# Kernel optimization log

Hardware: AMD Instinct MI355X
Metric: run time of the kernel (lower is better)

## Reference

```python
import jax, jax.numpy as jnp
import numpy as np

N, D_MODEL, D_PE, H = 4096, 512, 16, 8


def setup_inputs() -> dict:
    key = jax.random.key(0)
    ks = jax.random.split(key, 6)
    s = 1.0 / np.sqrt(D_MODEL)
    return {
        "x": jax.random.normal(ks[0], (N, D_MODEL), dtype=jnp.float32),
        "pe": jax.random.normal(ks[1], (N, D_PE), dtype=jnp.float32),
        "w_qkv": jax.random.normal(ks[2], (D_MODEL, 3 * D_MODEL), dtype=jnp.float32) * s,
        "b_qkv": jnp.zeros((3 * D_MODEL,), dtype=jnp.float32),
        "w_pe": jax.random.normal(ks[3], (D_PE, H), dtype=jnp.float32) * (1.0 / np.sqrt(D_PE)),
        "b_pe": jnp.zeros((H,), dtype=jnp.float32),
        "w_out": jax.random.normal(ks[4], (D_MODEL, D_MODEL), dtype=jnp.float32) * s,
        "b_out": jnp.zeros((D_MODEL,), dtype=jnp.float32),
    }


def reference(x, pe, w_qkv, b_qkv, w_pe, b_pe, w_out, b_out):
    n, d = x.shape
    h = w_pe.shape[1]
    hd = d // h
    scale = hd ** -0.5

    qkv = (x @ w_qkv + b_qkv).reshape(n, 3, h, hd)  # [N,3,H,hd]
    q = jnp.transpose(qkv[:, 0], (1, 0, 2))  # [H,N,hd]
    k = jnp.transpose(qkv[:, 1], (1, 0, 2))
    v = jnp.transpose(qkv[:, 2], (1, 0, 2))

    pe_proj = pe @ w_pe + b_pe  # [N,H]
    # bias[h,i,j] = pe_proj[j,h] - pe_proj[i,h]  (matches torch unsqueeze/permute)
    pt = pe_proj.T  # [H,N]
    bias = pt[:, None, :] - pt[:, :, None]  # [H,N,N]

    scores = jnp.einsum('hnd,hmd->hnm', q, k) * scale + bias  # [H,N,N]
    attn = jax.nn.softmax(scores, axis=-1)
    out = jnp.einsum('hnm,hmd->hnd', attn, v)  # [H,N,hd]
    out = jnp.transpose(out, (1, 0, 2)).reshape(n, d)
    return out @ w_out + b_out
```

## Files before the change

### kernel.cpp

```cpp
#include <hip/hip_runtime.h>
#include <stdint.h>
#include <stddef.h>


typedef unsigned short u16;
typedef __attribute__((ext_vector_type(8))) short short8;
typedef __attribute__((ext_vector_type(8))) unsigned short us8;
typedef __attribute__((ext_vector_type(4))) unsigned short us4;
typedef __attribute__((ext_vector_type(4))) float floatx4;

__device__ __forceinline__ u16 f2b(float f) {
  union { float f; uint32_t u; } v; v.f = f;
  uint32_t u = v.u;
  return (u16)((u + 0x7fffu + ((u >> 16) & 1u)) >> 16);
}

__device__ __forceinline__ uint32_t pkbf16(float a, float b) {
  union { float f; uint32_t u; } x, y; x.f = a; y.f = b;
  return __builtin_amdgcn_perm(y.u + 0x8000u, x.u + 0x8000u, 0x07060302u);
}

#if __has_builtin(__builtin_amdgcn_exp2f)
__device__ __forceinline__ float fexp2(float x) { return __builtin_amdgcn_exp2f(x); }
#else
__device__ __forceinline__ float fexp2(float x) { return exp2f(x); }
#endif

__device__ __forceinline__ void gld16(const u16* g, u16* l) {
  __builtin_amdgcn_global_load_lds(
      (const __attribute__((address_space(1))) uint32_t*)(const void*)g,
      (__attribute__((address_space(3))) uint32_t*)(void*)l, 16, 0, 0);
}


__device__ __forceinline__ void tr_tile(const float* __restrict__ in,
                                        u16* __restrict__ out, int R, int C,
                                        int bx, int by, u16 (*tile)[33]) {
  int tx = threadIdx.x & 31, ty = threadIdx.x >> 5;
  int c0 = bx * 32, r0 = by * 32;
#pragma unroll
  for (int i = 0; i < 32; i += 8)
    tile[ty + i][tx] = f2b(in[(size_t)(r0 + ty + i) * C + c0 + tx]);
  __syncthreads();
#pragma unroll
  for (int i = 0; i < 32; i += 8)
    out[(size_t)(c0 + ty + i) * R + r0 + tx] = tile[tx][ty + i];
}

__global__ __launch_bounds__(256) void k_prep(
    const float* __restrict__ x, u16* __restrict__ xb,
    const float* __restrict__ w_qkv, u16* __restrict__ wqkvT,
    const float* __restrict__ w_out, u16* __restrict__ woutT,
    const float* __restrict__ pe, const float* __restrict__ w_pe,
    const float* __restrict__ b_pe, float* __restrict__ peT) {
  __shared__ u16 tile[32][33];
  int b = blockIdx.x;
  if (b < 2048) {
    int i = b * 256 + threadIdx.x;
    float4 v = ((const float4*)x)[i];
    uint2 o = make_uint2(pkbf16(v.x, v.y), pkbf16(v.z, v.w));
    ((uint2*)xb)[i] = o;
  } else if (b < 2816) {
    int idx = b - 2048;
    tr_tile(w_qkv, wqkvT, 512, 1536, idx % 48, idx / 48, tile);
  } else if (b < 3072) {
    int idx = b - 2816;
    tr_tile(w_out, woutT, 512, 512, idx % 16, idx / 16, tile);
  } else {
    int idx = (b - 3072) * 256 + threadIdx.x;
    int h = idx >> 12, n = idx & 4095;
    float acc = b_pe[h];
#pragma unroll
    for (int d = 0; d < 16; ++d) acc = fmaf(pe[n * 16 + d], w_pe[d * 8 + h], acc);
    peT[h * 4096 + n] = acc * 1.4426950408889634f - 16.0f;
  }
}


__global__ __launch_bounds__(512, 6) void k_gemm_qkv(const u16* __restrict__ A,
                                                     const u16* __restrict__ Bt,
                                                     const float* __restrict__ bias,
                                                     u16* __restrict__ qk,
                                                     u16* __restrict__ vtp) {
  __shared__ __align__(16) u16 smem[24576];
  const int tid = threadIdx.x;
  const int lane = tid & 63, wave = tid >> 6;
  const int colx = lane & 15, quad = lane >> 4;
  const int m0 = blockIdx.y * 64, n0 = blockIdx.x * 128;
  const int wm = wave >> 2, wn = wave & 3;
  const int sc = (lane & 7) ^ ((lane >> 3) & 7);
  const floatx4 fz = {0.f, 0.f, 0.f, 0.f};
  floatx4 acc[2][2];
#pragma unroll
  for (int i = 0; i < 2; ++i)
#pragma unroll
    for (int j = 0; j < 2; ++j) acc[i][j] = fz;

#define PREF_QKV(k0, b)                                                       \
  {                                                                           \
    int rowa = wave * 8 + (lane >> 3);                                        \
    gld16(&A[(size_t)(m0 + rowa) * 512 + (k0) + sc * 8],                      \
          &smem[(b) * 4096 + wave * 512 + lane * 8]);                         \
    _Pragma("unroll") for (int c = 0; c < 2; ++c) {                           \
      int rowb = wave * 16 + c * 8 + (lane >> 3);                             \
      gld16(&Bt[(size_t)(n0 + rowb) * 512 + (k0) + sc * 8],                   \
            &smem[8192 + (b) * 8192 + wave * 1024 + c * 512 + lane * 8]);     \
    }                                                                         \
  }

  PREF_QKV(0, 0);
  __syncthreads();
  for (int it = 0; it < 8; ++it) {
    int cur = it & 1;
    if (it < 7) PREF_QKV((it + 1) * 64, cur ^ 1);
    const u16* As = &smem[cur * 4096];
    const u16* Bs = &smem[8192 + cur * 8192];
#pragma unroll
    for (int kk = 0; kk < 2; ++kk) {
      short8 af[2], bf[2];
#pragma unroll
      for (int i = 0; i < 2; ++i) {
        int row = wm * 32 + i * 16 + colx;
        af[i] = *(const short8*)&As[row * 64 + (((kk * 4 + quad) ^ (colx & 7))) * 8];
      }
#pragma unroll
      for (int j = 0; j < 2; ++j) {
        int row = wn * 32 + j * 16 + colx;
        bf[j] = *(const short8*)&Bs[row * 64 + (((kk * 4 + quad) ^ (colx & 7))) * 8];
      }
#pragma unroll
      for (int i = 0; i < 2; ++i)
#pragma unroll
        for (int j = 0; j < 2; ++j)
          acc[i][j] = __builtin_amdgcn_mfma_f32_16x16x32_bf16(af[i], bf[j], acc[i][j], 0, 0, 0);
    }
    __syncthreads();
  }

  const bool isV = (blockIdx.x >= 8);
#pragma unroll
  for (int j = 0; j < 2; ++j) {
    int c = n0 + wn * 32 + j * 16 + colx;
    float bq = bias[c];
    if (!isV) {
#pragma unroll
      for (int i = 0; i < 2; ++i)
#pragma unroll
        for (int r = 0; r < 4; ++r) {
          int row = m0 + wm * 32 + i * 16 + quad * 4 + r;
          qk[(size_t)row * 1024 + c] = f2b(acc[i][j][r] + bq);
        }
    } else {
      int d = c - 1024;
#pragma unroll
      for (int i = 0; i < 2; ++i) {
        us4 o;
#pragma unroll
        for (int r = 0; r < 4; ++r) o[r] = f2b(acc[i][j][r] + bq);
        *(us4*)&vtp[(size_t)d * 4096 + m0 + wm * 32 + quad * 8 + i * 4] = o;
      }
    }
  }
#undef PREF_QKV
}


__global__ __launch_bounds__(512, 4) void k_gemm_out(const u16* __restrict__ A,
                                                     const u16* __restrict__ Bt,
                                                     const float* __restrict__ bias,
                                                     float* __restrict__ Cout) {
  __shared__ __align__(16) u16 smem[16384];
  const int tid = threadIdx.x;
  const int lane = tid & 63, wave = tid >> 6;
  const int colx = lane & 15, quad = lane >> 4;
  const int m0 = blockIdx.y * 64, n0 = blockIdx.x * 64;
  const int wm = wave >> 2, wn = wave & 3;
  const int sc = (lane & 7) ^ ((lane >> 3) & 7);
  const floatx4 fz = {0.f, 0.f, 0.f, 0.f};
  floatx4 acc[2];
  acc[0] = fz; acc[1] = fz;

#define PREF_OUT(k0, b)                                                       \
  {                                                                           \
    int rowa = wave * 8 + (lane >> 3);                                        \
    gld16(&A[(size_t)(m0 + rowa) * 512 + (k0) + sc * 8],                      \
          &smem[(b) * 4096 + wave * 512 + lane * 8]);                         \
    gld16(&Bt[(size_t)(n0 + rowa) * 512 + (k0) + sc * 8],                     \
          &smem[8192 + (b) * 4096 + wave * 512 + lane * 8]);                  \
  }

  PREF_OUT(0, 0);
  __syncthreads();
  for (int it = 0; it < 8; ++it) {
    int cur = it & 1;
    if (it < 7) PREF_OUT((it + 1) * 64, cur ^ 1);
    const u16* As = &smem[cur * 4096];
    const u16* Bs = &smem[8192 + cur * 4096];
#pragma unroll
    for (int kk = 0; kk < 2; ++kk) {
      short8 af[2], bf;
#pragma unroll
      for (int i = 0; i < 2; ++i) {
        int row = wm * 32 + i * 16 + colx;
        af[i] = *(const short8*)&As[row * 64 + (((kk * 4 + quad) ^ (colx & 7))) * 8];
      }
      {
        int row = wn * 16 + colx;
        bf = *(const short8*)&Bs[row * 64 + (((kk * 4 + quad) ^ (colx & 7))) * 8];
      }
#pragma unroll
      for (int i = 0; i < 2; ++i)
        acc[i] = __builtin_amdgcn_mfma_f32_16x16x32_bf16(af[i], bf, acc[i], 0, 0, 0);
    }
    __syncthreads();
  }
  int c = n0 + wn * 16 + colx;
  float bq = bias[c];
#pragma unroll
  for (int i = 0; i < 2; ++i)
#pragma unroll
    for (int r = 0; r < 4; ++r) {
      int row = m0 + wm * 32 + i * 16 + quad * 4 + r;
      Cout[(size_t)row * 512 + c] = acc[i][r] + bq;
    }
#undef PREF_OUT
}


__global__ __launch_bounds__(512, 8) void k_flash(const u16* __restrict__ qk,
                                                  const u16* __restrict__ vt,
                                                  const float* __restrict__ peT,
                                                  float* __restrict__ opart,
                                                  float* __restrict__ lpart) {
  __shared__ __align__(16) u16 smem[20480];
  float* bufs = (float*)smem;

  const int tid = threadIdx.x;
  const int lane = tid & 63, wave = tid >> 6;
  const int colx = lane & 15, quad = lane >> 4;
  const int ih = wave >> 1, jq = wave & 1;
  const int q0 = blockIdx.x * 64;
  const int h = blockIdx.y;
  const int z = blockIdx.z;
  const int kvb = z * 2048;
  const float sscale = 0.125f * 1.4426950408889634f;
  const floatx4 fz = {0.f, 0.f, 0.f, 0.f};

  const int sc = (lane & 7) ^ ((lane >> 3) & 7);
  const int srow = wave * 8 + (lane >> 3);

#define PREF_F(j0n, b)                                                        \
  {                                                                           \
    gld16(&qk[(size_t)(kvb + (j0n) + srow) * 1024 + 512 + h * 64 + sc * 8],   \
          &smem[4096 + (b) * 4096 + wave * 512 + lane * 8]);                  \
    gld16(&vt[(size_t)(h * 64 + srow) * 4096 + kvb + (j0n) + sc * 8],         \
          &smem[12288 + (b) * 4096 + wave * 512 + lane * 8]);                 \
  }

  {
    int row = tid >> 3, ch = tid & 7;
    *(us8*)&smem[row * 64 + (ch ^ (row & 7)) * 8] =
        *(const us8*)&qk[(size_t)(q0 + row) * 1024 + h * 64 + ch * 8];
  }
  PREF_F(0, 0);
  __syncthreads();

  short8 qf[2];
#pragma unroll
  for (int kk = 0; kk < 2; ++kk) {
    int row = ih * 16 + colx;
    qf[kk] = *(const short8*)&smem[row * 64 + (((kk * 4 + quad) ^ (colx & 7))) * 8];
  }

  floatx4 oacc[4];
#pragma unroll
  for (int cb = 0; cb < 4; ++cb) oacc[cb] = fz;
  float rsum = 0.0f;

  for (int it = 0; it < 32; ++it) {
    const int cur = it & 1;
    if (it < 31) PREF_F((it + 1) * 64, cur ^ 1);
    const u16* Ks = &smem[4096 + cur * 4096];
    const u16* Vts = &smem[12288 + cur * 4096];

    floatx4 pev[2];
#pragma unroll
    for (int j2 = 0; j2 < 2; ++j2)
      pev[j2] = *(const floatx4*)&peT[h * 4096 + kvb + it * 64 + jq * 32 + j2 * 16 + quad * 4];

    floatx4 sacc[2] = {fz, fz};
#pragma unroll
    for (int j2 = 0; j2 < 2; ++j2) {
#pragma unroll
      for (int kk = 0; kk < 2; ++kk) {
        int row = jq * 32 + j2 * 16 + colx;
        short8 kf = *(const short8*)&Ks[row * 64 + (((kk * 4 + quad) ^ (colx & 7))) * 8];
        sacc[j2] = __builtin_amdgcn_mfma_f32_16x16x32_bf16(kf, qf[kk], sacc[j2], 0, 0, 0);
      }
    }
    union { uint32_t w[4]; short8 s; } pk;
#pragma unroll
    for (int j2 = 0; j2 < 2; ++j2) {
      float p0 = fexp2(fmaf(sacc[j2][0], sscale, pev[j2][0]));
      float p1 = fexp2(fmaf(sacc[j2][1], sscale, pev[j2][1]));
      float p2 = fexp2(fmaf(sacc[j2][2], sscale, pev[j2][2]));
      float p3 = fexp2(fmaf(sacc[j2][3], sscale, pev[j2][3]));
      rsum += (p0 + p1) + (p2 + p3);
      pk.w[j2 * 2 + 0] = pkbf16(p0, p1);
      pk.w[j2 * 2 + 1] = pkbf16(p2, p3);
    }
#pragma unroll
    for (int cb = 0; cb < 4; ++cb) {
      int row = cb * 16 + colx;
      short8 vf = *(const short8*)&Vts[row * 64 + (((jq * 4 + quad) ^ (colx & 7))) * 8];
      oacc[cb] = __builtin_amdgcn_mfma_f32_16x16x32_bf16(pk.s, vf, oacc[cb], 0, 0, 0);
    }
    __syncthreads();
  }

  rsum += __shfl_xor(rsum, 16);
  rsum += __shfl_xor(rsum, 32);

  float* b = bufs + ih * 1040;
  if (jq == 1) {
#pragma unroll
    for (int cb = 0; cb < 4; ++cb)
#pragma unroll
      for (int r = 0; r < 4; ++r)
        b[(quad * 4 + r) * 65 + cb * 16 + colx] = oacc[cb][r];
    if (quad == 0) b[colx * 65 + 64] = rsum;
  }
  __syncthreads();
  if (jq == 0) {
#pragma unroll
    for (int cb = 0; cb < 4; ++cb)
#pragma unroll
      for (int r = 0; r < 4; ++r)
        oacc[cb][r] += b[(quad * 4 + r) * 65 + cb * 16 + colx];
    rsum += b[colx * 65 + 64];
    float* op = opart + (size_t)z * 2097152;
#pragma unroll
    for (int cb = 0; cb < 4; ++cb)
#pragma unroll
      for (int r = 0; r < 4; ++r)
        op[(size_t)(q0 + ih * 16 + quad * 4 + r) * 512 + h * 64 + cb * 16 + colx] =
            oacc[cb][r];
    if (quad == 0)
      lpart[z * 32768 + h * 4096 + q0 + ih * 16 + colx] = rsum;
  }
#undef PREF_F
}


__global__ __launch_bounds__(256) void k_comb(const float* __restrict__ opart,
                                              const float* __restrict__ lpart,
                                              u16* __restrict__ ao) {
  int idx = blockIdx.x * 256 + threadIdx.x;
  int n = idx >> 7, d4 = idx & 127;
  int h = d4 >> 4;
  float l = lpart[h * 4096 + n] + lpart[32768 + h * 4096 + n];
  float inv = 1.0f / l;
  float4 o0 = *(const float4*)&opart[(size_t)n * 512 + d4 * 4];
  float4 o1 = *(const float4*)&opart[2097152 + (size_t)n * 512 + d4 * 4];
  us4 o;
  o[0] = f2b((o0.x + o1.x) * inv);
  o[1] = f2b((o0.y + o1.y) * inv);
  o[2] = f2b((o0.z + o1.z) * inv);
  o[3] = f2b((o0.w + o1.w) * inv);
  *(us4*)&ao[(size_t)n * 512 + d4 * 4] = o;
}


extern "C" void kernel_launch(void* const* d_in, const int* in_sizes, int n_in,
                              void* d_out, int out_size, void* d_ws, size_t ws_size,
                              hipStream_t stream) {
  const float* x     = (const float*)d_in[0];
  const float* pe    = (const float*)d_in[1];
  const float* w_qkv = (const float*)d_in[2];
  const float* b_qkv = (const float*)d_in[3];
  const float* w_pe  = (const float*)d_in[4];
  const float* b_pe  = (const float*)d_in[5];
  const float* w_out = (const float*)d_in[6];
  const float* b_out = (const float*)d_in[7];
  float* out = (float*)d_out;

  u16* xb    = (u16*)d_ws;
  u16* wqkvT = xb    + 2097152;
  u16* woutT = wqkvT + 786432;
  u16* qk    = woutT + 262144;
  u16* vt    = qk    + 4194304;
  u16* ao    = vt    + 2097152;
  float* peT   = (float*)(ao + 2097152);
  float* opart = peT + 32768;
  float* lpart = opart + 4194304;

  k_prep<<<3200, 256, 0, stream>>>(x, xb, w_qkv, wqkvT, w_out, woutT,
                                   pe, w_pe, b_pe, peT);
  k_gemm_qkv<<<dim3(12, 64), 512, 0, stream>>>(xb, wqkvT, b_qkv, qk, vt);
  k_flash<<<dim3(64, 8, 2), 512, 0, stream>>>(qk, vt, peT, opart, lpart);
  k_comb<<<2048, 256, 0, stream>>>(opart, lpart, ao);
  k_gemm_out<<<dim3(8, 64), 512, 0, stream>>>(ao, woutT, b_out, out);
}
```

Baseline: 152.5 us.

## Switch flash kernel to 32x32x16 MFMA with 4 waves and prescaled Q

```diff
diff --git a/kernel.cpp b/kernel.cpp
--- a/kernel.cpp
+++ b/kernel.cpp
@@ -8,6 +8,7 @@
 typedef __attribute__((ext_vector_type(8))) unsigned short us8;
 typedef __attribute__((ext_vector_type(4))) unsigned short us4;
 typedef __attribute__((ext_vector_type(4))) float floatx4;
+typedef __attribute__((ext_vector_type(16))) float floatx16;
 
 __device__ __forceinline__ u16 f2b(float f) {
   union { float f; uint32_t u; } v; v.f = f;
@@ -30,6 +31,13 @@
   __builtin_amdgcn_global_load_lds(
       (const __attribute__((address_space(1))) uint32_t*)(const void*)g,
       (__attribute__((address_space(3))) uint32_t*)(void*)l, 16, 0, 0);
+}
+
+__device__ __forceinline__ floatx16 zero16() {
+  floatx16 v;
+#pragma unroll
+  for (int i = 0; i < 16; ++i) v[i] = 0.0f;
+  return v;
 }
 
 
@@ -138,17 +146,19 @@
   }
 
   const bool isV = (blockIdx.x >= 8);
+  const int qsw = ((quad & 1) << 1) | (quad >> 1);
 #pragma unroll
   for (int j = 0; j < 2; ++j) {
     int c = n0 + wn * 32 + j * 16 + colx;
     float bq = bias[c];
     if (!isV) {
+      float qs = (c < 512) ? 0.18033688011112042f : 1.0f;
 #pragma unroll
       for (int i = 0; i < 2; ++i)
 #pragma unroll
         for (int r = 0; r < 4; ++r) {
           int row = m0 + wm * 32 + i * 16 + quad * 4 + r;
-          qk[(size_t)row * 1024 + c] = f2b(acc[i][j][r] + bq);
+          qk[(size_t)row * 1024 + c] = f2b((acc[i][j][r] + bq) * qs);
         }
     } else {
       int d = c - 1024;
@@ -157,7 +167,7 @@
         us4 o;
 #pragma unroll
         for (int r = 0; r < 4; ++r) o[r] = f2b(acc[i][j][r] + bq);
-        *(us4*)&vtp[(size_t)d * 4096 + m0 + wm * 32 + quad * 8 + i * 4] = o;
+        *(us4*)&vtp[(size_t)d * 4096 + m0 + wm * 32 + i * 16 + qsw * 4] = o;
       }
     }
   }
@@ -165,69 +175,7 @@
 }
 
 
-__global__ __launch_bounds__(512, 4) void k_gemm_out(const u16* __restrict__ A,
-                                                     const u16* __restrict__ Bt,
-                                                     const float* __restrict__ bias,
-                                                     float* __restrict__ Cout) {
-  __shared__ __align__(16) u16 smem[16384];
-  const int tid = threadIdx.x;
-  const int lane = tid & 63, wave = tid >> 6;
-  const int colx = lane & 15, quad = lane >> 4;
-  const int m0 = blockIdx.y * 64, n0 = blockIdx.x * 64;
-  const int wm = wave >> 2, wn = wave & 3;
-  const int sc = (lane & 7) ^ ((lane >> 3) & 7);
-  const floatx4 fz = {0.f, 0.f, 0.f, 0.f};
-  floatx4 acc[2];
-  acc[0] = fz; acc[1] = fz;
-
-#define PREF_OUT(k0, b)                                                       \
-  {                                                                           \
-    int rowa = wave * 8 + (lane >> 3);                                        \
-    gld16(&A[(size_t)(m0 + rowa) * 512 + (k0) + sc * 8],                      \
-          &smem[(b) * 4096 + wave * 512 + lane * 8]);                         \
-    gld16(&Bt[(size_t)(n0 + rowa) * 512 + (k0) + sc * 8],                     \
-          &smem[8192 + (b) * 4096 + wave * 512 + lane * 8]);                  \
-  }
-
-  PREF_OUT(0, 0);
-  __syncthreads();
-  for (int it = 0; it < 8; ++it) {
-    int cur = it & 1;
-    if (it < 7) PREF_OUT((it + 1) * 64, cur ^ 1);
-    const u16* As = &smem[cur * 4096];
-    const u16* Bs = &smem[8192 + cur * 4096];
-#pragma unroll
-    for (int kk = 0; kk < 2; ++kk) {
-      short8 af[2], bf;
-#pragma unroll
-      for (int i = 0; i < 2; ++i) {
-        int row = wm * 32 + i * 16 + colx;
-        af[i] = *(const short8*)&As[row * 64 + (((kk * 4 + quad) ^ (colx & 7))) * 8];
-      }
-      {
-        int row = wn * 16 + colx;
-        bf = *(const short8*)&Bs[row * 64 + (((kk * 4 + quad) ^ (colx & 7))) * 8];
-      }
-#pragma unroll
-      for (int i = 0; i < 2; ++i)
-        acc[i] = __builtin_amdgcn_mfma_f32_16x16x32_bf16(af[i], bf, acc[i], 0, 0, 0);
-    }
-    __syncthreads();
-  }
-  int c = n0 + wn * 16 + colx;
-  float bq = bias[c];
-#pragma unroll
-  for (int i = 0; i < 2; ++i)
-#pragma unroll
-    for (int r = 0; r < 4; ++r) {
-      int row = m0 + wm * 32 + i * 16 + quad * 4 + r;
-      Cout[(size_t)row * 512 + c] = acc[i][r] + bq;
-    }
-#undef PREF_OUT
-}
-
-
-__global__ __launch_bounds__(512, 8) void k_flash(const u16* __restrict__ qk,
+__global__ __launch_bounds__(256, 4) void k_flash(const u16* __restrict__ qk,
                                                   const u16* __restrict__ vt,
                                                   const float* __restrict__ peT,
                                                   float* __restrict__ opart,
@@ -237,118 +185,138 @@
 
   const int tid = threadIdx.x;
   const int lane = tid & 63, wave = tid >> 6;
-  const int colx = lane & 15, quad = lane >> 4;
+  const int n31 = lane & 31, L = lane >> 5;
   const int ih = wave >> 1, jq = wave & 1;
   const int q0 = blockIdx.x * 64;
   const int h = blockIdx.y;
   const int z = blockIdx.z;
   const int kvb = z * 2048;
-  const float sscale = 0.125f * 1.4426950408889634f;
-  const floatx4 fz = {0.f, 0.f, 0.f, 0.f};
 
   const int sc = (lane & 7) ^ ((lane >> 3) & 7);
-  const int srow = wave * 8 + (lane >> 3);
-
-#define PREF_F(j0n, b)                                                        \
-  {                                                                           \
-    gld16(&qk[(size_t)(kvb + (j0n) + srow) * 1024 + 512 + h * 64 + sc * 8],   \
-          &smem[4096 + (b) * 4096 + wave * 512 + lane * 8]);                  \
-    gld16(&vt[(size_t)(h * 64 + srow) * 4096 + kvb + (j0n) + sc * 8],         \
-          &smem[12288 + (b) * 4096 + wave * 512 + lane * 8]);                 \
-  }
-
-  {
-    int row = tid >> 3, ch = tid & 7;
+  const int sr = lane >> 3;
+
+#pragma unroll
+  for (int rr = 0; rr < 2; ++rr) {
+    int idx = rr * 256 + tid;
+    int row = idx >> 3, ch = idx & 7;
     *(us8*)&smem[row * 64 + (ch ^ (row & 7)) * 8] =
         *(const us8*)&qk[(size_t)(q0 + row) * 1024 + h * 64 + ch * 8];
   }
-  PREF_F(0, 0);
+  const u16* qptr = qk + (size_t)kvb * 1024 + 512 + h * 64 + sc * 8;
+  const u16* vptr = vt + (size_t)(h * 64) * 4096 + kvb + sc * 8;
+#pragma unroll
+  for (int rr = 0; rr < 2; ++rr) {
+    int row = rr * 32 + wave * 8 + sr;
+    gld16(qptr + (size_t)row * 1024, &smem[4096 + rr * 2048 + wave * 512 + lane * 8]);
+    gld16(vptr + (size_t)row * 4096, &smem[12288 + rr * 2048 + wave * 512 + lane * 8]);
+  }
+  qptr += 65536;
+  vptr += 64;
+  const float* pptr = peT + h * 4096 + kvb + jq * 32 + 4 * L;
   __syncthreads();
 
-  short8 qf[2];
-#pragma unroll
-  for (int kk = 0; kk < 2; ++kk) {
-    int row = ih * 16 + colx;
-    qf[kk] = *(const short8*)&smem[row * 64 + (((kk * 4 + quad) ^ (colx & 7))) * 8];
-  }
-
-  floatx4 oacc[4];
-#pragma unroll
-  for (int cb = 0; cb < 4; ++cb) oacc[cb] = fz;
+  short8 qf[4];
+  {
+    int row = ih * 32 + n31, r7 = row & 7;
+#pragma unroll
+    for (int dc = 0; dc < 4; ++dc)
+      qf[dc] = *(const short8*)&smem[row * 64 + (((dc * 2 + L) ^ r7)) * 8];
+  }
+
+  floatx16 oacc0 = zero16(), oacc1 = zero16();
   float rsum = 0.0f;
 
   for (int it = 0; it < 32; ++it) {
     const int cur = it & 1;
-    if (it < 31) PREF_F((it + 1) * 64, cur ^ 1);
+    floatx4 pev[4];
+#pragma unroll
+    for (int c4 = 0; c4 < 4; ++c4)
+      pev[c4] = *(const floatx4*)(pptr + c4 * 8);
+    pptr += 64;
+    if (it < 31) {
+#pragma unroll
+      for (int rr = 0; rr < 2; ++rr) {
+        int row = rr * 32 + wave * 8 + sr;
+        gld16(qptr + (size_t)row * 1024,
+              &smem[4096 + (cur ^ 1) * 4096 + rr * 2048 + wave * 512 + lane * 8]);
+        gld16(vptr + (size_t)row * 4096,
+              &smem[12288 + (cur ^ 1) * 4096 + rr * 2048 + wave * 512 + lane * 8]);
+      }
+      qptr += 65536;
+      vptr += 64;
+    }
     const u16* Ks = &smem[4096 + cur * 4096];
     const u16* Vts = &smem[12288 + cur * 4096];
 
-    floatx4 pev[2];
-#pragma unroll
-    for (int j2 = 0; j2 < 2; ++j2)
-      pev[j2] = *(const floatx4*)&peT[h * 4096 + kvb + it * 64 + jq * 32 + j2 * 16 + quad * 4];
-
-    floatx4 sacc[2] = {fz, fz};
-#pragma unroll
-    for (int j2 = 0; j2 < 2; ++j2) {
-#pragma unroll
-      for (int kk = 0; kk < 2; ++kk) {
-        int row = jq * 32 + j2 * 16 + colx;
-        short8 kf = *(const short8*)&Ks[row * 64 + (((kk * 4 + quad) ^ (colx & 7))) * 8];
-        sacc[j2] = __builtin_amdgcn_mfma_f32_16x16x32_bf16(kf, qf[kk], sacc[j2], 0, 0, 0);
-      }
-    }
-    union { uint32_t w[4]; short8 s; } pk;
-#pragma unroll
-    for (int j2 = 0; j2 < 2; ++j2) {
-      float p0 = fexp2(fmaf(sacc[j2][0], sscale, pev[j2][0]));
-      float p1 = fexp2(fmaf(sacc[j2][1], sscale, pev[j2][1]));
-      float p2 = fexp2(fmaf(sacc[j2][2], sscale, pev[j2][2]));
-      float p3 = fexp2(fmaf(sacc[j2][3], sscale, pev[j2][3]));
+    floatx16 sacc = zero16();
+    {
+      int row = jq * 32 + n31, r7 = row & 7;
+#pragma unroll
+      for (int dc = 0; dc < 4; ++dc) {
+        short8 kf = *(const short8*)&Ks[row * 64 + (((dc * 2 + L) ^ r7)) * 8];
+        sacc = __builtin_amdgcn_mfma_f32_32x32x16_bf16(kf, qf[dc], sacc, 0, 0, 0);
+      }
+    }
+    union { uint32_t w[8]; short8 s[2]; } pk;
+#pragma unroll
+    for (int c4 = 0; c4 < 4; ++c4) {
+      float p0 = fexp2(sacc[c4 * 4 + 0] + pev[c4][0]);
+      float p1 = fexp2(sacc[c4 * 4 + 1] + pev[c4][1]);
+      float p2 = fexp2(sacc[c4 * 4 + 2] + pev[c4][2]);
+      float p3 = fexp2(sacc[c4 * 4 + 3] + pev[c4][3]);
       rsum += (p0 + p1) + (p2 + p3);
-      pk.w[j2 * 2 + 0] = pkbf16(p0, p1);
-      pk.w[j2 * 2 + 1] = pkbf16(p2, p3);
-    }
-#pragma unroll
-    for (int cb = 0; cb < 4; ++cb) {
-      int row = cb * 16 + colx;
-      short8 vf = *(const short8*)&Vts[row * 64 + (((jq * 4 + quad) ^ (colx & 7))) * 8];
-      oacc[cb] = __builtin_amdgcn_mfma_f32_16x16x32_bf16(pk.s, vf, oacc[cb], 0, 0, 0);
+      pk.w[c4 * 2 + 0] = pkbf16(p0, p1);
+      pk.w[c4 * 2 + 1] = pkbf16(p2, p3);
+    }
+#pragma unroll
+    for (int m01 = 0; m01 < 2; ++m01) {
+      int ch = jq * 4 + m01 * 2 + L;
+      {
+        int row = n31, r7 = row & 7;
+        short8 vf = *(const short8*)&Vts[row * 64 + ((ch ^ r7)) * 8];
+        oacc0 = __builtin_amdgcn_mfma_f32_32x32x16_bf16(pk.s[m01], vf, oacc0, 0, 0, 0);
+      }
+      {
+        int row = 32 + n31, r7 = row & 7;
+        short8 vf = *(const short8*)&Vts[row * 64 + ((ch ^ r7)) * 8];
+        oacc1 = __builtin_amdgcn_mfma_f32_32x32x16_bf16(pk.s[m01], vf, oacc1, 0, 0, 0);
+      }
     }
     __syncthreads();
   }
 
-  rsum += __shfl_xor(rsum, 16);
   rsum += __shfl_xor(rsum, 32);
 
-  float* b = bufs + ih * 1040;
+  float* b = bufs + ih * 2080;
   if (jq == 1) {
 #pragma unroll
-    for (int cb = 0; cb < 4; ++cb)
-#pragma unroll
-      for (int r = 0; r < 4; ++r)
-        b[(quad * 4 + r) * 65 + cb * 16 + colx] = oacc[cb][r];
-    if (quad == 0) b[colx * 65 + 64] = rsum;
+    for (int reg = 0; reg < 16; ++reg) {
+      int qr = (reg & 3) + 8 * (reg >> 2) + 4 * L;
+      b[qr * 65 + n31] = oacc0[reg];
+      b[qr * 65 + 32 + n31] = oacc1[reg];
+    }
+    if (L == 0) b[n31 * 65 + 64] = rsum;
   }
   __syncthreads();
   if (jq == 0) {
 #pragma unroll
-    for (int cb = 0; cb < 4; ++cb)
-#pragma unroll
-      for (int r = 0; r < 4; ++r)
-        oacc[cb][r] += b[(quad * 4 + r) * 65 + cb * 16 + colx];
-    rsum += b[colx * 65 + 64];
+    for (int reg = 0; reg < 16; ++reg) {
+      int qr = (reg & 3) + 8 * (reg >> 2) + 4 * L;
+      oacc0[reg] += b[qr * 65 + n31];
+      oacc1[reg] += b[qr * 65 + 32 + n31];
+    }
+    rsum += b[n31 * 65 + 64];
     float* op = opart + (size_t)z * 2097152;
 #pragma unroll
-    for (int cb = 0; cb < 4; ++cb)
-#pragma unroll
-      for (int r = 0; r < 4; ++r)
-        op[(size_t)(q0 + ih * 16 + quad * 4 + r) * 512 + h * 64 + cb * 16 + colx] =
-            oacc[cb][r];
-    if (quad == 0)
-      lpart[z * 32768 + h * 4096 + q0 + ih * 16 + colx] = rsum;
-  }
-#undef PREF_F
+    for (int reg = 0; reg < 16; ++reg) {
+      int qr = (reg & 3) + 8 * (reg >> 2) + 4 * L;
+      size_t base = (size_t)(q0 + ih * 32 + qr) * 512 + h * 64;
+      op[base + n31] = oacc0[reg];
+      op[base + 32 + n31] = oacc1[reg];
+    }
+    if (L == 0)
+      lpart[z * 32768 + h * 4096 + q0 + ih * 32 + n31] = rsum;
+  }
 }
 
 
@@ -371,6 +339,68 @@
 }
 
 
+__global__ __launch_bounds__(512, 4) void k_gemm_out(const u16* __restrict__ A,
+                                                     const u16* __restrict__ Bt,
+                                                     const float* __restrict__ bias,
+                                                     float* __restrict__ Cout) {
+  __shared__ __align__(16) u16 smem[16384];
+  const int tid = threadIdx.x;
+  const int lane = tid & 63, wave = tid >> 6;
+  const int colx = lane & 15, quad = lane >> 4;
+  const int m0 = blockIdx.y * 64, n0 = blockIdx.x * 64;
+  const int wm = wave >> 2, wn = wave & 3;
+  const int sc = (lane & 7) ^ ((lane >> 3) & 7);
+  const floatx4 fz = {0.f, 0.f, 0.f, 0.f};
+  floatx4 acc[2];
+  acc[0] = fz; acc[1] = fz;
+
+#define PREF_OUT(k0, b)                                                       \
+  {                                                                           \
+    int rowa = wave * 8 + (lane >> 3);                                        \
+    gld16(&A[(size_t)(m0 + rowa) * 512 + (k0) + sc * 8],                      \
+          &smem[(b) * 4096 + wave * 512 + lane * 8]);                         \
+    gld16(&Bt[(size_t)(n0 + rowa) * 512 + (k0) + sc * 8],                     \
+          &smem[8192 + (b) * 4096 + wave * 512 + lane * 8]);                  \
+  }
+
+  PREF_OUT(0, 0);
+  __syncthreads();
+  for (int it = 0; it < 8; ++it) {
+    int cur = it & 1;
+    if (it < 7) PREF_OUT((it + 1) * 64, cur ^ 1);
+    const u16* As = &smem[cur * 4096];
+    const u16* Bs = &smem[8192 + cur * 4096];
+#pragma unroll
+    for (int kk = 0; kk < 2; ++kk) {
+      short8 af[2], bf;
+#pragma unroll
+      for (int i = 0; i < 2; ++i) {
+        int row = wm * 32 + i * 16 + colx;
+        af[i] = *(const short8*)&As[row * 64 + (((kk * 4 + quad) ^ (colx & 7))) * 8];
+      }
+      {
+        int row = wn * 16 + colx;
+        bf = *(const short8*)&Bs[row * 64 + (((kk * 4 + quad) ^ (colx & 7))) * 8];
+      }
+#pragma unroll
+      for (int i = 0; i < 2; ++i)
+        acc[i] = __builtin_amdgcn_mfma_f32_16x16x32_bf16(af[i], bf, acc[i], 0, 0, 0);
+    }
+    __syncthreads();
+  }
+  int c = n0 + wn * 16 + colx;
+  float bq = bias[c];
+#pragma unroll
+  for (int i = 0; i < 2; ++i)
+#pragma unroll
+    for (int r = 0; r < 4; ++r) {
+      int row = m0 + wm * 32 + i * 16 + quad * 4 + r;
+      Cout[(size_t)row * 512 + c] = acc[i][r] + bq;
+    }
+#undef PREF_OUT
+}
+
+
 extern "C" void kernel_launch(void* const* d_in, const int* in_sizes, int n_in,
                               void* d_out, int out_size, void* d_ws, size_t ws_size,
                               hipStream_t stream) {
@@ -397,7 +427,7 @@
   k_prep<<<3200, 256, 0, stream>>>(x, xb, w_qkv, wqkvT, w_out, woutT,
                                    pe, w_pe, b_pe, peT);
   k_gemm_qkv<<<dim3(12, 64), 512, 0, stream>>>(xb, wqkvT, b_qkv, qk, vt);
-  k_flash<<<dim3(64, 8, 2), 512, 0, stream>>>(qk, vt, peT, opart, lpart);
+  k_flash<<<dim3(64, 8, 2), 256, 0, stream>>>(qk, vt, peT, opart, lpart);
   k_comb<<<2048, 256, 0, stream>>>(opart, lpart, ao);
   k_gemm_out<<<dim3(8, 64), 512, 0, stream>>>(ao, woutT, b_out, out);
 }
```

Result: slower. 157.3 us (+3.1%).
